# Optimization experiments

Measured on AMD Instinct MI355X. Metric: run time of the kernel, lower is better.

Reference implementation:

```python
import jax, jax.numpy as jnp
import numpy as np

TOP_K = 8
NUM_GROUPS = 8


def setup_inputs() -> dict:
    key = jax.random.key(0)
    ks = jax.random.split(key, 6)
    T_B, T_S, H, I, E, G = 1, 2048, 2048, 768, 32, NUM_GROUPS
    hidden_states = jax.random.normal(ks[0], (T_B, T_S, H), dtype=jnp.float32)
    gate_weight = jax.random.normal(ks[1], (E, H), dtype=jnp.float32) * 0.02
    gate_up_proj = jax.random.normal(ks[2], (E, 2 * I, H), dtype=jnp.float32) * 0.02
    down_proj = jax.random.normal(ks[3], (E, H, I), dtype=jnp.float32) * 0.02
    merge_groups = jax.random.randint(ks[4], (E,), 0, G, dtype=jnp.int64)
    # ensure every group id appears at least once so dominant experts are well-defined
    merge_groups = merge_groups.at[:G].set(jnp.arange(G, dtype=jnp.int64))
    dominant_experts = jax.random.randint(ks[5], (G,), 0, E, dtype=jnp.int64)
    return {
        "hidden_states": hidden_states,
        "gate_weight": gate_weight,
        "gate_up_proj": gate_up_proj,
        "down_proj": down_proj,
        "merge_groups": merge_groups,
        "dominant_experts": dominant_experts,
    }


def reference(hidden_states, gate_weight, gate_up_proj, down_proj, merge_groups, dominant_experts):
    B, S, H = hidden_states.shape
    G = dominant_experts.shape[0]
    x = hidden_states.reshape(-1, H)  # [T, H]

    # Router: softmax over all experts, then top-k of the probabilities (as in source)
    logits = jnp.einsum("th,eh->te", x, gate_weight)
    probs = jax.nn.softmax(logits.astype(jnp.float32), axis=-1).astype(logits.dtype)
    top_val, top_idx = jax.lax.top_k(probs, TOP_K)  # [T, K]
    top_val = top_val / jnp.sum(top_val, axis=-1, keepdims=True)  # norm_topk_prob

    # Each selected expert e is replaced by its group's dominant expert; by linearity
    # of the scatter-add combine, sum routing weights per (token, group).
    sel_group = merge_groups[top_idx]  # [T, K] in [0, G)
    onehot = jax.nn.one_hot(sel_group, G, dtype=top_val.dtype)  # [T, K, G]
    w_tg = jnp.einsum("tk,tkg->tg", top_val, onehot)  # combined weight per token/group

    gu = gate_up_proj[dominant_experts]  # [G, 2I, H]
    dn = down_proj[dominant_experts]     # [G, H, I]

    h = jnp.einsum("th,goh->tgo", x, gu)           # [T, G, 2I]
    gate, up = jnp.split(h, 2, axis=-1)              # [T, G, I] each
    act = jax.nn.silu(gate) * up                     # SwiGLU
    y = jnp.einsum("tgi,ghi->tgh", act, dn)        # [T, G, H]
    out = jnp.einsum("tg,tgh->th", w_tg, y)        # combine
    return out.reshape(B, S, H)
```

## Files before the change

### kernel.cpp

```cpp
#include <hip/hip_runtime.h>
#include <hip/hip_bf16.h>

typedef __attribute__((ext_vector_type(8))) short short8v;
typedef __attribute__((ext_vector_type(4))) float f32x4;

#define T_TOK 2048
#define HDIM  2048
#define IDIM  768
#define NEXP  32
#define NGRP  8

__device__ __forceinline__ unsigned short f2b(float f){
  unsigned u = __float_as_uint(f);
  u = u + 0x7FFFu + ((u >> 16) & 1u);
  return (unsigned short)(u >> 16);
}
__device__ __forceinline__ float b2f(unsigned short s){
  return __uint_as_float(((unsigned)s) << 16);
}

__global__ __launch_bounds__(256) void router_kernel(
    const float* __restrict__ x, const float* __restrict__ gw,
    const int* __restrict__ mg, float* __restrict__ wtg,
    unsigned short* __restrict__ xb)
{
  __shared__ float xs[4][2048];
  __shared__ float lg[4][32];
  int tid = threadIdx.x;
  int t0 = blockIdx.x * 4;

  #pragma unroll
  for (int k = 0; k < 8; k++){
    int idx = k*256 + tid;
    int tok = idx >> 9, wi = idx & 511;
    float4 v = ((const float4*)(x + (size_t)(t0 + tok)*HDIM))[wi];
    ((float4*)xs[tok])[wi] = v;
    ushort4 b; b.x=f2b(v.x); b.y=f2b(v.y); b.z=f2b(v.z); b.w=f2b(v.w);
    ((ushort4*)(xb + (size_t)(t0+tok)*HDIM))[wi] = b;
  }
  __syncthreads();

  int e = tid >> 3, ch = tid & 7;
  float s0=0.f, s1=0.f, s2=0.f, s3=0.f;
  const float4* gv = (const float4*)(gw + (size_t)e*HDIM);
  #pragma unroll 4
  for (int k = 0; k < 64; k++){
    int i4 = ch + 8*k;
    float4 b  = gv[i4];
    float4 a0 = ((const float4*)xs[0])[i4];
    float4 a1 = ((const float4*)xs[1])[i4];
    float4 a2 = ((const float4*)xs[2])[i4];
    float4 a3 = ((const float4*)xs[3])[i4];
    s0 += a0.x*b.x + a0.y*b.y + a0.z*b.z + a0.w*b.w;
    s1 += a1.x*b.x + a1.y*b.y + a1.z*b.z + a1.w*b.w;
    s2 += a2.x*b.x + a2.y*b.y + a2.z*b.z + a2.w*b.w;
    s3 += a3.x*b.x + a3.y*b.y + a3.z*b.z + a3.w*b.w;
  }
  #pragma unroll
  for (int off=1; off<8; off<<=1){
    s0 += __shfl_xor(s0, off); s1 += __shfl_xor(s1, off);
    s2 += __shfl_xor(s2, off); s3 += __shfl_xor(s3, off);
  }
  if (ch == 0){ lg[0][e]=s0; lg[1][e]=s1; lg[2][e]=s2; lg[3][e]=s3; }
  __syncthreads();

  int wv = tid >> 6, lane = tid & 63;
  float val = (lane < 32) ? lg[wv][lane] : -1e30f;
  float mx = val;
  #pragma unroll
  for (int off=16; off; off>>=1) mx = fmaxf(mx, __shfl_xor(mx, off));
  float p = (lane < 32) ? expf(val - mx) : 0.f;
  float sm = p;
  #pragma unroll
  for (int off=16; off; off>>=1) sm += __shfl_xor(sm, off);
  float v = (lane < 32) ? (p / sm) : -1.f;
  int idx = lane;
  float vals[8]; int idxs[8];
  #pragma unroll
  for (int it=0; it<8; it++){
    float bv = v; int bi = idx;
    #pragma unroll
    for (int off=32; off; off>>=1){
      float ov = __shfl_xor(bv, off); int oi = __shfl_xor(bi, off);
      if (ov > bv || (ov == bv && oi < bi)){ bv = ov; bi = oi; }
    }
    vals[it] = bv; idxs[it] = bi;
    if (lane == bi) v = -1.f;
  }
  float tot = vals[0]+vals[1]+vals[2]+vals[3]+vals[4]+vals[5]+vals[6]+vals[7];
  float racc = 0.f;
  #pragma unroll
  for (int it=0; it<8; it++){
    int grp = mg[idxs[it]];
    if (lane == grp) racc += vals[it] / tot;
  }
  if (lane < 8) wtg[(size_t)(t0+wv)*NGRP + lane] = racc;
}

__global__ __launch_bounds__(256) void convert_kernel(
    const float* __restrict__ src, unsigned short* __restrict__ dst,
    const int* __restrict__ de, size_t per_expert)
{
  int g = blockIdx.z;
  size_t i4 = (size_t)blockIdx.x*256 + threadIdx.x;
  const float4* s = (const float4*)(src + (size_t)de[g]*per_expert);
  float4 vv = s[i4];
  ushort4 b; b.x=f2b(vv.x); b.y=f2b(vv.y); b.z=f2b(vv.z); b.w=f2b(vv.w);
  ((ushort4*)(dst + (size_t)g*per_expert))[i4] = b;
}

__device__ __forceinline__ void stage128x32(const unsigned short* g,
                                            int ld, unsigned short* lds, int tid)
{
  int w = tid >> 6;
  const unsigned short* g0 = g + (size_t)(tid >> 2)*ld + (tid & 3)*8;
  const unsigned short* g1 = g0 + (size_t)64*ld;
  __builtin_amdgcn_global_load_lds((const __attribute__((address_space(1))) void*)g0,
      (__attribute__((address_space(3))) void*)(lds + w*512), 16, 0, 0);
  __builtin_amdgcn_global_load_lds((const __attribute__((address_space(1))) void*)g1,
      (__attribute__((address_space(3))) void*)(lds + 2048 + w*512), 16, 0, 0);
}

__device__ __forceinline__ void frag_mma(const unsigned short* As,
                                         const unsigned short* Bs,
                                         f32x4 acc[4][4], int lane, int wr, int wc)
{
  int fr = lane & 15, kk = (lane >> 4) * 8;
  short8v a[4], b[4];
  #pragma unroll
  for (int m=0;m<4;m++) a[m] = *(const short8v*)(As + (wr*64 + m*16 + fr)*32 + kk);
  #pragma unroll
  for (int n=0;n<4;n++) b[n] = *(const short8v*)(Bs + (wc*64 + n*16 + fr)*32 + kk);
  #pragma unroll
  for (int m=0;m<4;m++){
    #pragma unroll
    for (int n=0;n<4;n++){
      acc[m][n] = __builtin_amdgcn_mfma_f32_16x16x32_bf16(a[m], b[n], acc[m][n], 0, 0, 0);
    }
  }
}

__global__ __launch_bounds__(256, 2) void gemm1_kernel(
    const unsigned short* __restrict__ xb, const unsigned short* __restrict__ gu,
    unsigned short* __restrict__ hb)
{
  __shared__ unsigned short As[4096], Bs[4096];
  int tid = threadIdx.x, lane = tid & 63, w = tid >> 6, wr = w >> 1, wc = w & 1;
  int m0 = blockIdx.x*128, n0 = blockIdx.y*128, g = blockIdx.z;
  const unsigned short* Ab = xb + (size_t)m0*HDIM;
  const unsigned short* Bb = gu + ((size_t)g*1536 + n0)*HDIM;
  f32x4 zero = {0.f,0.f,0.f,0.f};
  f32x4 acc[4][4];
  #pragma unroll
  for (int m=0;m<4;m++){ acc[m][0]=zero; acc[m][1]=zero; acc[m][2]=zero; acc[m][3]=zero; }
  for (int k0=0; k0<HDIM; k0+=32){
    __syncthreads();
    stage128x32(Ab + k0, HDIM, As, tid);
    stage128x32(Bb + k0, HDIM, Bs, tid);
    __syncthreads();
    frag_mma(As, Bs, acc, lane, wr, wc);
  }
  int col = lane & 15, r0 = (lane >> 4) * 4;
  unsigned short* C = hb + (size_t)g*T_TOK*1536;
  #pragma unroll
  for (int m=0;m<4;m++){
    int row = m0 + wr*64 + m*16 + r0;
    #pragma unroll
    for (int n=0;n<4;n++){
      int cc = n0 + wc*64 + n*16 + col;
      #pragma unroll
      for (int j=0;j<4;j++) C[(size_t)(row + j)*1536 + cc] = f2b(acc[m][n][j]);
    }
  }
}

__global__ __launch_bounds__(256) void swiglu_kernel(
    const unsigned short* __restrict__ hb, const float* __restrict__ wtg,
    unsigned short* __restrict__ actb)
{
  int cid = blockIdx.x*256 + threadIdx.x;
  int g = cid / 196608;
  int rem = cid - g*196608;
  int t = rem / 96;
  int c = rem - t*96;
  const unsigned short* row = hb + ((size_t)g*T_TOK + t)*1536;
  short8v g8 = *(const short8v*)(row + c*8);
  short8v u8 = *(const short8v*)(row + 768 + c*8);
  float wv = wtg[(size_t)t*NGRP + g];
  short8v r;
  #pragma unroll
  for (int j=0;j<8;j++){
    float gf = b2f((unsigned short)g8[j]);
    float uf = b2f((unsigned short)u8[j]);
    float sg = gf / (1.f + expf(-gf));
    r[j] = (short)f2b(sg * uf * wv);
  }
  *(short8v*)(actb + ((size_t)g*T_TOK + t)*IDIM + c*8) = r;
}

__global__ __launch_bounds__(256, 2) void gemm2_kernel(
    const unsigned short* __restrict__ actb, const unsigned short* __restrict__ dnb,
    float* __restrict__ part)
{
  __shared__ unsigned short As[4096], Bs[4096];
  int tid = threadIdx.x, lane = tid & 63, w = tid >> 6, wr = w >> 1, wc = w & 1;
  int m0 = blockIdx.x*128, n0 = blockIdx.y*128, z = blockIdx.z;
  f32x4 zero = {0.f,0.f,0.f,0.f};
  f32x4 acc[4][4];
  #pragma unroll
  for (int m=0;m<4;m++){ acc[m][0]=zero; acc[m][1]=zero; acc[m][2]=zero; acc[m][3]=zero; }
  for (int gg=0; gg<2; gg++){
    int g = z*2 + gg;
    const unsigned short* Ab = actb + ((size_t)g*T_TOK + m0)*IDIM;
    const unsigned short* Bb = dnb  + ((size_t)g*HDIM  + n0)*IDIM;
    for (int k0=0; k0<IDIM; k0+=32){
      __syncthreads();
      stage128x32(Ab + k0, IDIM, As, tid);
      stage128x32(Bb + k0, IDIM, Bs, tid);
      __syncthreads();
      frag_mma(As, Bs, acc, lane, wr, wc);
    }
  }
  int col = lane & 15, r0 = (lane >> 4) * 4;
  float* C = part + (size_t)z*T_TOK*HDIM;
  #pragma unroll
  for (int m=0;m<4;m++){
    int row = m0 + wr*64 + m*16 + r0;
    #pragma unroll
    for (int n=0;n<4;n++){
      int cc = n0 + wc*64 + n*16 + col;
      #pragma unroll
      for (int j=0;j<4;j++) C[(size_t)(row + j)*HDIM + cc] = acc[m][n][j];
    }
  }
}

__global__ __launch_bounds__(256) void reduce_kernel(
    const float* __restrict__ p, float* __restrict__ o)
{
  size_t i = ((size_t)blockIdx.x*256 + threadIdx.x)*4;
  float4 a0 = *(const float4*)(p + i);
  float4 a1 = *(const float4*)(p + 4194304 + i);
  float4 a2 = *(const float4*)(p + 8388608 + i);
  float4 a3 = *(const float4*)(p + 12582912 + i);
  float4 r;
  r.x = a0.x + a1.x + a2.x + a3.x;
  r.y = a0.y + a1.y + a2.y + a3.y;
  r.z = a0.z + a1.z + a2.z + a3.z;
  r.w = a0.w + a1.w + a2.w + a3.w;
  *(float4*)(o + i) = r;
}

extern "C" void kernel_launch(void* const* d_in, const int* in_sizes, int n_in,
                              void* d_out, int out_size, void* d_ws, size_t ws_size,
                              hipStream_t stream)
{
  (void)in_sizes; (void)n_in; (void)out_size; (void)ws_size;
  const float* x   = (const float*)d_in[0];
  const float* gw  = (const float*)d_in[1];
  const float* gup = (const float*)d_in[2];
  const float* dnp = (const float*)d_in[3];
  const int*   mg  = (const int*)d_in[4];
  const int*   de  = (const int*)d_in[5];
  float* out = (float*)d_out;
  char* ws = (char*)d_ws;

  float*          wtg  = (float*)(ws + 0);
  unsigned short* xb   = (unsigned short*)(ws + 65536);
  unsigned short* dnb  = (unsigned short*)(ws + 8454144);
  unsigned short* actb = (unsigned short*)(ws + 33619968);
  unsigned short* gub  = (unsigned short*)(ws + 58785792);
  unsigned short* hb   = (unsigned short*)(ws + 109117440);
  float*          part = (float*)(ws + 58785792);

  router_kernel<<<512, 256, 0, stream>>>(x, gw, mg, wtg, xb);
  convert_kernel<<<dim3(3072,1,8), 256, 0, stream>>>(gup, gub, de, (size_t)1536*2048);
  convert_kernel<<<dim3(1536,1,8), 256, 0, stream>>>(dnp, dnb, de, (size_t)2048*768);
  gemm1_kernel<<<dim3(16,12,8), 256, 0, stream>>>(xb, gub, hb);
  swiglu_kernel<<<6144, 256, 0, stream>>>(hb, wtg, actb);
  gemm2_kernel<<<dim3(16,16,4), 256, 0, stream>>>(actb, dnb, part);
  reduce_kernel<<<4096, 256, 0, stream>>>(part, out);
}
```

Before: 287.9 us.

## Rewrite both GEMMs as 256x256-tile double-buffered pipelined kernels with swizzled LDS

Both expert GEMMs move from 128x128 tiles with a K step of 32 and full syncs to 256x256 tiles with 8 waves and a K step of 64. The LDS is double-buffered and XOR-swizzled, and global-to-LDS loads for the next K-tile are interleaved across four MFMA phases using vmcnt waits and raw barriers, with s_setprio raised around MFMA bursts. The aim is to hide global load latency, cut LDS bank conflicts and raise arithmetic intensity per block. The trade-off is 128 KB of LDS per block, which makes the declared 2 blocks per CU unlikely, 128 accumulator registers per thread, and far fewer blocks (384 for gemm1 and 256 for gemm2), which could underfill 256 CUs.

```diff
diff --git a/kernel.cpp b/kernel.cpp
--- a/kernel.cpp
+++ b/kernel.cpp
@@ -109,67 +109,155 @@
   ((ushort4*)(dst + (size_t)g*per_expert))[i4] = b;
 }
 
-__device__ __forceinline__ void stage128x32(const unsigned short* g,
-                                            int ld, unsigned short* lds, int tid)
-{
-  int w = tid >> 6;
-  const unsigned short* g0 = g + (size_t)(tid >> 2)*ld + (tid & 3)*8;
-  const unsigned short* g1 = g0 + (size_t)64*ld;
-  __builtin_amdgcn_global_load_lds((const __attribute__((address_space(1))) void*)g0,
-      (__attribute__((address_space(3))) void*)(lds + w*512), 16, 0, 0);
-  __builtin_amdgcn_global_load_lds((const __attribute__((address_space(1))) void*)g1,
-      (__attribute__((address_space(3))) void*)(lds + 2048 + w*512), 16, 0, 0);
-}
-
-__device__ __forceinline__ void frag_mma(const unsigned short* As,
-                                         const unsigned short* Bs,
-                                         f32x4 acc[4][4], int lane, int wr, int wc)
-{
-  int fr = lane & 15, kk = (lane >> 4) * 8;
-  short8v a[4], b[4];
-  #pragma unroll
-  for (int m=0;m<4;m++) a[m] = *(const short8v*)(As + (wr*64 + m*16 + fr)*32 + kk);
-  #pragma unroll
-  for (int n=0;n<4;n++) b[n] = *(const short8v*)(Bs + (wc*64 + n*16 + fr)*32 + kk);
-  #pragma unroll
-  for (int m=0;m<4;m++){
+
+__device__ __forceinline__ void stage_half_g(
+    const unsigned short* __restrict__ gsrc, int ldElems,
+    unsigned short* __restrict__ ldsHalf, int tid)
+{
+  int rl0 = tid >> 3;
+  int cb  = (tid & 7) * 16;
+  int w   = tid >> 6;
+  #pragma unroll
+  for (int j = 0; j < 2; j++){
+    int rl  = j*64 + rl0;
+    int scb = cb ^ ((rl & 4) << 3);
+    const unsigned short* src = gsrc + (size_t)rl*ldElems + (scb >> 1);
+    __builtin_amdgcn_global_load_lds(
+        (const __attribute__((address_space(1))) void*)src,
+        (__attribute__((address_space(3))) void*)(ldsHalf + j*4096 + w*512),
+        16, 0, 0);
+  }
+}
+
+template<int P>
+__device__ __forceinline__ void read_a_frags(const unsigned short* Ab,
+                                             short8v (&a)[4][2], int fr, int colOff)
+{
+  #pragma unroll
+  for (int i=0;i<4;i++){
+    const char* rb = (const char*)Ab + (size_t)(((P*4+i)*16 + fr)*128);
+    a[i][0] = *(const short8v*)(rb + colOff);
+    a[i][1] = *(const short8v*)(rb + 64 + colOff);
+  }
+}
+
+__device__ __forceinline__ void read_b_frags(const unsigned short* Bb,
+                                             short8v (&b)[2][2], int wn, int fr, int colOff)
+{
+  #pragma unroll
+  for (int n=0;n<2;n++){
+    const char* rb = (const char*)Bb + (size_t)((wn*32 + n*16 + fr)*128);
+    b[n][0] = *(const short8v*)(rb + colOff);
+    b[n][1] = *(const short8v*)(rb + 64 + colOff);
+  }
+}
+
+template<int P>
+__device__ __forceinline__ void mfma_phase(const short8v (&a)[4][2],
+                                           const short8v (&b)[2][2],
+                                           f32x4 (&acc)[16][2])
+{
+  __builtin_amdgcn_s_setprio(1);
+  #pragma unroll
+  for (int i=0;i<4;i++){
     #pragma unroll
-    for (int n=0;n<4;n++){
-      acc[m][n] = __builtin_amdgcn_mfma_f32_16x16x32_bf16(a[m], b[n], acc[m][n], 0, 0, 0);
+    for (int n=0;n<2;n++){
+      acc[P*4+i][n] = __builtin_amdgcn_mfma_f32_16x16x32_bf16(a[i][0], b[n][0], acc[P*4+i][n], 0,0,0);
+      acc[P*4+i][n] = __builtin_amdgcn_mfma_f32_16x16x32_bf16(a[i][1], b[n][1], acc[P*4+i][n], 0,0,0);
     }
   }
-}
-
-__global__ __launch_bounds__(256, 2) void gemm1_kernel(
+  __builtin_amdgcn_s_setprio(0);
+}
+
+#define BARRIER() do { __builtin_amdgcn_s_barrier(); __builtin_amdgcn_sched_barrier(0); } while(0)
+#define WAITV(N)  asm volatile("s_waitcnt vmcnt(" #N ")" ::: "memory")
+
+__global__ __launch_bounds__(512, 2) void gemm1_kernel(
     const unsigned short* __restrict__ xb, const unsigned short* __restrict__ gu,
     unsigned short* __restrict__ hb)
 {
-  __shared__ unsigned short As[4096], Bs[4096];
-  int tid = threadIdx.x, lane = tid & 63, w = tid >> 6, wr = w >> 1, wc = w & 1;
-  int m0 = blockIdx.x*128, n0 = blockIdx.y*128, g = blockIdx.z;
-  const unsigned short* Ab = xb + (size_t)m0*HDIM;
-  const unsigned short* Bb = gu + ((size_t)g*1536 + n0)*HDIM;
-  f32x4 zero = {0.f,0.f,0.f,0.f};
-  f32x4 acc[4][4];
-  #pragma unroll
-  for (int m=0;m<4;m++){ acc[m][0]=zero; acc[m][1]=zero; acc[m][2]=zero; acc[m][3]=zero; }
-  for (int k0=0; k0<HDIM; k0+=32){
-    __syncthreads();
-    stage128x32(Ab + k0, HDIM, As, tid);
-    stage128x32(Bb + k0, HDIM, Bs, tid);
-    __syncthreads();
-    frag_mma(As, Bs, acc, lane, wr, wc);
-  }
-  int col = lane & 15, r0 = (lane >> 4) * 4;
-  unsigned short* C = hb + (size_t)g*T_TOK*1536;
-  #pragma unroll
-  for (int m=0;m<4;m++){
-    int row = m0 + wr*64 + m*16 + r0;
+  __shared__ unsigned short Al[2][16384];
+  __shared__ unsigned short Bl[2][16384];
+  int tid = threadIdx.x, lane = tid & 63, wn = tid >> 6;
+  int fr = lane & 15;
+  int colOff = ((lane >> 4) * 16) ^ ((lane & 4) << 3);
+  int m0 = blockIdx.x * 256, n0 = blockIdx.y * 256, g = blockIdx.z;
+  const unsigned short* Abase = xb + (size_t)m0 * HDIM;
+  const unsigned short* Bbase = gu + ((size_t)g * 1536 + n0) * HDIM;
+
+  f32x4 acc[16][2];
+  #pragma unroll
+  for (int m=0;m<16;m++){ acc[m][0] = (f32x4){0,0,0,0}; acc[m][1] = (f32x4){0,0,0,0}; }
+  short8v bfrag[2][2];
+
+  #define STG1(buf, unit, kt2) do { \
+    if ((unit)==0)      stage_half_g(Bbase + (size_t)(kt2)*64,                   HDIM, &Bl[buf][0],    tid); \
+    else if ((unit)==1) stage_half_g(Bbase + (size_t)128*HDIM + (size_t)(kt2)*64,HDIM, &Bl[buf][8192], tid); \
+    else if ((unit)==2) stage_half_g(Abase + (size_t)(kt2)*64,                   HDIM, &Al[buf][0],    tid); \
+    else                stage_half_g(Abase + (size_t)128*HDIM + (size_t)(kt2)*64,HDIM, &Al[buf][8192], tid); \
+  } while(0)
+
+  STG1(0,0,0); STG1(0,1,0); STG1(0,2,0); STG1(0,3,0);
+  WAITV(3);
+  BARRIER();
+
+  for (int kt = 0; kt < 31; ++kt){
+    const unsigned short* Ab = Al[kt & 1];
+    const unsigned short* Bb = Bl[kt & 1];
+    int nb = (kt + 1) & 1, k2 = kt + 1;
+    { short8v a[4][2]; read_a_frags<0>(Ab, a, fr, colOff);
+      read_b_frags(Bb, bfrag, wn, fr, colOff);
+      STG1(nb, 0, k2);
+      WAITV(4); BARRIER();
+      mfma_phase<0>(a, bfrag, acc);
+      BARRIER(); }
+    { short8v a[4][2]; read_a_frags<1>(Ab, a, fr, colOff);
+      STG1(nb, 1, k2);
+      WAITV(5); BARRIER();
+      mfma_phase<1>(a, bfrag, acc);
+      BARRIER(); }
+    { short8v a[4][2]; read_a_frags<2>(Ab, a, fr, colOff);
+      STG1(nb, 2, k2);
+      WAITV(6); BARRIER();
+      mfma_phase<2>(a, bfrag, acc);
+      BARRIER(); }
+    { short8v a[4][2]; read_a_frags<3>(Ab, a, fr, colOff);
+      STG1(nb, 3, k2);
+      WAITV(3); BARRIER();
+      mfma_phase<3>(a, bfrag, acc);
+      BARRIER(); }
+  }
+  {
+    const unsigned short* Ab = Al[1];
+    const unsigned short* Bb = Bl[1];
+    { short8v a[4][2]; read_a_frags<0>(Ab, a, fr, colOff);
+      read_b_frags(Bb, bfrag, wn, fr, colOff);
+      WAITV(2); BARRIER();
+      mfma_phase<0>(a, bfrag, acc);
+      BARRIER(); }
+    { short8v a[4][2]; read_a_frags<1>(Ab, a, fr, colOff);
+      WAITV(1); BARRIER();
+      mfma_phase<1>(a, bfrag, acc);
+      BARRIER(); }
+    { short8v a[4][2]; read_a_frags<2>(Ab, a, fr, colOff);
+      WAITV(0); BARRIER();
+      mfma_phase<2>(a, bfrag, acc);
+      BARRIER(); }
+    { short8v a[4][2]; read_a_frags<3>(Ab, a, fr, colOff);
+      mfma_phase<3>(a, bfrag, acc); }
+  }
+  #undef STG1
+
+  unsigned short* Cb = hb + (size_t)g * T_TOK * 1536;
+  int r0 = (lane >> 4) * 4, c0 = n0 + wn * 32 + fr;
+  #pragma unroll
+  for (int m = 0; m < 16; m++){
     #pragma unroll
-    for (int n=0;n<4;n++){
-      int cc = n0 + wc*64 + n*16 + col;
+    for (int n = 0; n < 2; n++){
       #pragma unroll
-      for (int j=0;j<4;j++) C[(size_t)(row + j)*1536 + cc] = f2b(acc[m][n][j]);
+      for (int j = 0; j < 4; j++){
+        Cb[(size_t)(m0 + m*16 + r0 + j) * 1536 + (c0 + n*16)] = f2b(acc[m][n][j]);
+      }
     }
   }
 }
@@ -198,39 +286,95 @@
   *(short8v*)(actb + ((size_t)g*T_TOK + t)*IDIM + c*8) = r;
 }
 
-__global__ __launch_bounds__(256, 2) void gemm2_kernel(
+__global__ __launch_bounds__(512, 2) void gemm2_kernel(
     const unsigned short* __restrict__ actb, const unsigned short* __restrict__ dnb,
     float* __restrict__ part)
 {
-  __shared__ unsigned short As[4096], Bs[4096];
-  int tid = threadIdx.x, lane = tid & 63, w = tid >> 6, wr = w >> 1, wc = w & 1;
-  int m0 = blockIdx.x*128, n0 = blockIdx.y*128, z = blockIdx.z;
-  f32x4 zero = {0.f,0.f,0.f,0.f};
-  f32x4 acc[4][4];
-  #pragma unroll
-  for (int m=0;m<4;m++){ acc[m][0]=zero; acc[m][1]=zero; acc[m][2]=zero; acc[m][3]=zero; }
-  for (int gg=0; gg<2; gg++){
-    int g = z*2 + gg;
-    const unsigned short* Ab = actb + ((size_t)g*T_TOK + m0)*IDIM;
-    const unsigned short* Bb = dnb  + ((size_t)g*HDIM  + n0)*IDIM;
-    for (int k0=0; k0<IDIM; k0+=32){
-      __syncthreads();
-      stage128x32(Ab + k0, IDIM, As, tid);
-      stage128x32(Bb + k0, IDIM, Bs, tid);
-      __syncthreads();
-      frag_mma(As, Bs, acc, lane, wr, wc);
-    }
-  }
-  int col = lane & 15, r0 = (lane >> 4) * 4;
-  float* C = part + (size_t)z*T_TOK*HDIM;
-  #pragma unroll
-  for (int m=0;m<4;m++){
-    int row = m0 + wr*64 + m*16 + r0;
+  __shared__ unsigned short Al[2][16384];
+  __shared__ unsigned short Bl[2][16384];
+  int tid = threadIdx.x, lane = tid & 63, wn = tid >> 6;
+  int fr = lane & 15;
+  int colOff = ((lane >> 4) * 16) ^ ((lane & 4) << 3);
+  int m0 = blockIdx.x * 256, n0 = blockIdx.y * 256, z = blockIdx.z;
+
+  f32x4 acc[16][2];
+  #pragma unroll
+  for (int m=0;m<16;m++){ acc[m][0] = (f32x4){0,0,0,0}; acc[m][1] = (f32x4){0,0,0,0}; }
+  short8v bfrag[2][2];
+
+  #define STG2(buf, unit, kt2) do { \
+    int gi = ((kt2) >= 12) ? 1 : 0; \
+    int gg = z*2 + gi; \
+    int kk = ((kt2) - gi*12) * 64; \
+    const unsigned short* Aseg = actb + (size_t)(gg*T_TOK + m0)*IDIM + kk; \
+    const unsigned short* Bseg = dnb  + (size_t)(gg*HDIM + n0)*IDIM + kk; \
+    if ((unit)==0)      stage_half_g(Bseg,                      IDIM, &Bl[buf][0],    tid); \
+    else if ((unit)==1) stage_half_g(Bseg + (size_t)128*IDIM,   IDIM, &Bl[buf][8192], tid); \
+    else if ((unit)==2) stage_half_g(Aseg,                      IDIM, &Al[buf][0],    tid); \
+    else                stage_half_g(Aseg + (size_t)128*IDIM,   IDIM, &Al[buf][8192], tid); \
+  } while(0)
+
+  STG2(0,0,0); STG2(0,1,0); STG2(0,2,0); STG2(0,3,0);
+  WAITV(3);
+  BARRIER();
+
+  for (int kt = 0; kt < 23; ++kt){
+    const unsigned short* Ab = Al[kt & 1];
+    const unsigned short* Bb = Bl[kt & 1];
+    int nb = (kt + 1) & 1, k2 = kt + 1;
+    { short8v a[4][2]; read_a_frags<0>(Ab, a, fr, colOff);
+      read_b_frags(Bb, bfrag, wn, fr, colOff);
+      STG2(nb, 0, k2);
+      WAITV(4); BARRIER();
+      mfma_phase<0>(a, bfrag, acc);
+      BARRIER(); }
+    { short8v a[4][2]; read_a_frags<1>(Ab, a, fr, colOff);
+      STG2(nb, 1, k2);
+      WAITV(5); BARRIER();
+      mfma_phase<1>(a, bfrag, acc);
+      BARRIER(); }
+    { short8v a[4][2]; read_a_frags<2>(Ab, a, fr, colOff);
+      STG2(nb, 2, k2);
+      WAITV(6); BARRIER();
+      mfma_phase<2>(a, bfrag, acc);
+      BARRIER(); }
+    { short8v a[4][2]; read_a_frags<3>(Ab, a, fr, colOff);
+      STG2(nb, 3, k2);
+      WAITV(3); BARRIER();
+      mfma_phase<3>(a, bfrag, acc);
+      BARRIER(); }
+  }
+  {
+    const unsigned short* Ab = Al[1];
+    const unsigned short* Bb = Bl[1];
+    { short8v a[4][2]; read_a_frags<0>(Ab, a, fr, colOff);
+      read_b_frags(Bb, bfrag, wn, fr, colOff);
+      WAITV(2); BARRIER();
+      mfma_phase<0>(a, bfrag, acc);
+      BARRIER(); }
+    { short8v a[4][2]; read_a_frags<1>(Ab, a, fr, colOff);
+      WAITV(1); BARRIER();
+      mfma_phase<1>(a, bfrag, acc);
+      BARRIER(); }
+    { short8v a[4][2]; read_a_frags<2>(Ab, a, fr, colOff);
+      WAITV(0); BARRIER();
+      mfma_phase<2>(a, bfrag, acc);
+      BARRIER(); }
+    { short8v a[4][2]; read_a_frags<3>(Ab, a, fr, colOff);
+      mfma_phase<3>(a, bfrag, acc); }
+  }
+  #undef STG2
+
+  float* Cb = part + (size_t)z * T_TOK * HDIM;
+  int r0 = (lane >> 4) * 4, c0 = n0 + wn * 32 + fr;
+  #pragma unroll
+  for (int m = 0; m < 16; m++){
     #pragma unroll
-    for (int n=0;n<4;n++){
-      int cc = n0 + wc*64 + n*16 + col;
+    for (int n = 0; n < 2; n++){
       #pragma unroll
-      for (int j=0;j<4;j++) C[(size_t)(row + j)*HDIM + cc] = acc[m][n][j];
+      for (int j = 0; j < 4; j++){
+        Cb[(size_t)(m0 + m*16 + r0 + j) * HDIM + (c0 + n*16)] = acc[m][n][j];
+      }
     }
   }
 }
@@ -276,8 +420,8 @@
   router_kernel<<<512, 256, 0, stream>>>(x, gw, mg, wtg, xb);
   convert_kernel<<<dim3(3072,1,8), 256, 0, stream>>>(gup, gub, de, (size_t)1536*2048);
   convert_kernel<<<dim3(1536,1,8), 256, 0, stream>>>(dnp, dnb, de, (size_t)2048*768);
-  gemm1_kernel<<<dim3(16,12,8), 256, 0, stream>>>(xb, gub, hb);
+  gemm1_kernel<<<dim3(8,6,8), 512, 0, stream>>>(xb, gub, hb);
   swiglu_kernel<<<6144, 256, 0, stream>>>(hb, wtg, actb);
-  gemm2_kernel<<<dim3(16,16,4), 256, 0, stream>>>(actb, dnb, part);
+  gemm2_kernel<<<dim3(8,8,4), 512, 0, stream>>>(actb, dnb, part);
   reduce_kernel<<<4096, 256, 0, stream>>>(part, out);
 }
```

After: 287.1 us. Within noise of the previous version (-0.3%).

## Fuse SwiGLU into gemm1 epilogue and rewrite GEMMs with double-buffered 256x256 tiles

Applied to the files above, without the earlier changes.

The gate/up weight conversion now interleaves gate and up rows in 16-row chunks, so each gemm1 tile holds matching gate and up columns. This lets SwiGLU and the routing weight be applied in the gemm1 epilogue, which removes the intermediate hb tensor and the separate swiglu kernel. Both GEMMs move to 512-thread blocks with 256x256 tiles, 64-wide K steps, XOR-swizzled LDS, double-buffered global-to-LDS loads overlapped with MFMA, and raised wave priority around the MFMA sections. The cost is higher register and LDS use per block and fewer blocks in the grid, which may limit occupancy.

```diff
diff --git a/kernel.cpp b/kernel.cpp
--- a/kernel.cpp
+++ b/kernel.cpp
@@ -7,7 +7,6 @@
 #define T_TOK 2048
 #define HDIM  2048
 #define IDIM  768
-#define NEXP  32
 #define NGRP  8
 
 __device__ __forceinline__ unsigned short f2b(float f){
@@ -97,140 +96,234 @@
   if (lane < 8) wtg[(size_t)(t0+wv)*NGRP + lane] = racc;
 }
 
-__global__ __launch_bounds__(256) void convert_kernel(
+__global__ __launch_bounds__(256) void convert_gu_kernel(
     const float* __restrict__ src, unsigned short* __restrict__ dst,
-    const int* __restrict__ de, size_t per_expert)
+    const int* __restrict__ de)
+{
+  int g = blockIdx.z;
+  int i4 = blockIdx.x*256 + threadIdx.x;
+  int j  = i4 >> 9;
+  int c4 = i4 & 511;
+  int q = j >> 5, r = j & 31;
+  int srow = (r < 16) ? (q*16 + r) : (768 + q*16 + (r - 16));
+  const float4* s = (const float4*)(src + ((size_t)de[g]*1536 + srow)*HDIM);
+  float4 vv = s[c4];
+  ushort4 b; b.x=f2b(vv.x); b.y=f2b(vv.y); b.z=f2b(vv.z); b.w=f2b(vv.w);
+  ((ushort4*)(dst + ((size_t)g*1536 + j)*HDIM))[c4] = b;
+}
+
+__global__ __launch_bounds__(256) void convert_dn_kernel(
+    const float* __restrict__ src, unsigned short* __restrict__ dst,
+    const int* __restrict__ de)
 {
   int g = blockIdx.z;
   size_t i4 = (size_t)blockIdx.x*256 + threadIdx.x;
-  const float4* s = (const float4*)(src + (size_t)de[g]*per_expert);
+  const float4* s = (const float4*)(src + (size_t)de[g]*1572864);
   float4 vv = s[i4];
   ushort4 b; b.x=f2b(vv.x); b.y=f2b(vv.y); b.z=f2b(vv.z); b.w=f2b(vv.w);
-  ((ushort4*)(dst + (size_t)g*per_expert))[i4] = b;
-}
-
-__device__ __forceinline__ void stage128x32(const unsigned short* g,
-                                            int ld, unsigned short* lds, int tid)
-{
-  int w = tid >> 6;
-  const unsigned short* g0 = g + (size_t)(tid >> 2)*ld + (tid & 3)*8;
-  const unsigned short* g1 = g0 + (size_t)64*ld;
-  __builtin_amdgcn_global_load_lds((const __attribute__((address_space(1))) void*)g0,
-      (__attribute__((address_space(3))) void*)(lds + w*512), 16, 0, 0);
-  __builtin_amdgcn_global_load_lds((const __attribute__((address_space(1))) void*)g1,
-      (__attribute__((address_space(3))) void*)(lds + 2048 + w*512), 16, 0, 0);
-}
-
-__device__ __forceinline__ void frag_mma(const unsigned short* As,
-                                         const unsigned short* Bs,
-                                         f32x4 acc[4][4], int lane, int wr, int wc)
-{
-  int fr = lane & 15, kk = (lane >> 4) * 8;
-  short8v a[4], b[4];
-  #pragma unroll
-  for (int m=0;m<4;m++) a[m] = *(const short8v*)(As + (wr*64 + m*16 + fr)*32 + kk);
-  #pragma unroll
-  for (int n=0;n<4;n++) b[n] = *(const short8v*)(Bs + (wc*64 + n*16 + fr)*32 + kk);
-  #pragma unroll
-  for (int m=0;m<4;m++){
+  ((ushort4*)(dst + (size_t)g*1572864))[i4] = b;
+}
+
+
+__device__ __forceinline__ void stage_half_g(
+    const unsigned short* __restrict__ gsrc, int ldElems,
+    unsigned short* __restrict__ ldsHalf, int tid)
+{
+  int rl0 = tid >> 3;
+  int cb  = (tid & 7) * 16;
+  int w   = tid >> 6;
+  #pragma unroll
+  for (int j = 0; j < 2; j++){
+    int rl  = j*64 + rl0;
+    int scb = cb ^ ((rl & 7) << 4);
+    const unsigned short* src = gsrc + (size_t)rl*ldElems + (scb >> 1);
+    __builtin_amdgcn_global_load_lds(
+        (const __attribute__((address_space(1))) void*)src,
+        (__attribute__((address_space(3))) void*)(ldsHalf + j*4096 + w*512),
+        16, 0, 0);
+  }
+}
+
+__device__ __forceinline__ void read_b4(const unsigned short* Bb,
+                                        short8v (&b)[4][2], int wn, int fr, int colOff)
+{
+  #pragma unroll
+  for (int n=0;n<4;n++){
+    const char* rb = (const char*)Bb + (size_t)((wn*64 + n*16 + fr)*128);
+    b[n][0] = *(const short8v*)(rb + colOff);
+    b[n][1] = *(const short8v*)(rb + (colOff ^ 64));
+  }
+}
+
+template<int P>
+__device__ __forceinline__ void subphase(const unsigned short* Ab, int wm, int fr, int colOff,
+                                         const short8v (&b)[4][2], f32x4 (&acc)[8][4])
+{
+  short8v a[2][2];
+  #pragma unroll
+  for (int i=0;i<2;i++){
+    const char* rb = (const char*)Ab + (size_t)((wm*128 + (P*2+i)*16 + fr)*128);
+    a[i][0] = *(const short8v*)(rb + colOff);
+    a[i][1] = *(const short8v*)(rb + (colOff ^ 64));
+  }
+  __builtin_amdgcn_s_setprio(1);
+  #pragma unroll
+  for (int i=0;i<2;i++){
     #pragma unroll
     for (int n=0;n<4;n++){
-      acc[m][n] = __builtin_amdgcn_mfma_f32_16x16x32_bf16(a[m], b[n], acc[m][n], 0, 0, 0);
+      acc[P*2+i][n] = __builtin_amdgcn_mfma_f32_16x16x32_bf16(a[i][0], b[n][0], acc[P*2+i][n],0,0,0);
+      acc[P*2+i][n] = __builtin_amdgcn_mfma_f32_16x16x32_bf16(a[i][1], b[n][1], acc[P*2+i][n],0,0,0);
     }
   }
-}
-
-__global__ __launch_bounds__(256, 2) void gemm1_kernel(
+  __builtin_amdgcn_s_setprio(0);
+}
+
+#define WAITV(N)  asm volatile("s_waitcnt vmcnt(" #N ")" ::: "memory")
+
+__global__ __launch_bounds__(512, 2) void gemm1_kernel(
     const unsigned short* __restrict__ xb, const unsigned short* __restrict__ gu,
-    unsigned short* __restrict__ hb)
-{
-  __shared__ unsigned short As[4096], Bs[4096];
-  int tid = threadIdx.x, lane = tid & 63, w = tid >> 6, wr = w >> 1, wc = w & 1;
-  int m0 = blockIdx.x*128, n0 = blockIdx.y*128, g = blockIdx.z;
-  const unsigned short* Ab = xb + (size_t)m0*HDIM;
-  const unsigned short* Bb = gu + ((size_t)g*1536 + n0)*HDIM;
-  f32x4 zero = {0.f,0.f,0.f,0.f};
-  f32x4 acc[4][4];
-  #pragma unroll
-  for (int m=0;m<4;m++){ acc[m][0]=zero; acc[m][1]=zero; acc[m][2]=zero; acc[m][3]=zero; }
-  for (int k0=0; k0<HDIM; k0+=32){
-    __syncthreads();
-    stage128x32(Ab + k0, HDIM, As, tid);
-    stage128x32(Bb + k0, HDIM, Bs, tid);
-    __syncthreads();
-    frag_mma(As, Bs, acc, lane, wr, wc);
-  }
-  int col = lane & 15, r0 = (lane >> 4) * 4;
-  unsigned short* C = hb + (size_t)g*T_TOK*1536;
-  #pragma unroll
-  for (int m=0;m<4;m++){
-    int row = m0 + wr*64 + m*16 + r0;
-    #pragma unroll
-    for (int n=0;n<4;n++){
-      int cc = n0 + wc*64 + n*16 + col;
+    const float* __restrict__ wtg, unsigned short* __restrict__ actb)
+{
+  __shared__ unsigned short Al[2][16384];
+  __shared__ unsigned short Bl[2][16384];
+  int tid = threadIdx.x, lane = tid & 63, w = tid >> 6;
+  int wm = w >> 2, wn = w & 3;
+  int fr = lane & 15;
+  int colOff = ((lane >> 4) * 16) ^ ((fr & 7) << 4);
+  int bid = blockIdx.x;
+  int P = bid % 48, mb = bid / 48;
+  int m0 = mb * 256, n0 = (P % 6) * 256, g = P / 6;
+  const unsigned short* Abase = xb + (size_t)m0 * HDIM;
+  const unsigned short* Bbase = gu + ((size_t)g * 1536 + n0) * HDIM;
+
+  f32x4 acc[8][4];
+  #pragma unroll
+  for (int m=0;m<8;m++){
+    #pragma unroll
+    for (int n=0;n<4;n++) acc[m][n] = (f32x4){0,0,0,0};
+  }
+  short8v b[4][2];
+
+  #define STG1(buf, kt2) do { \
+    stage_half_g(Bbase + (size_t)(kt2)*64,                    HDIM, &Bl[buf][0],    tid); \
+    stage_half_g(Bbase + (size_t)128*HDIM + (size_t)(kt2)*64, HDIM, &Bl[buf][8192], tid); \
+    stage_half_g(Abase + (size_t)(kt2)*64,                    HDIM, &Al[buf][0],    tid); \
+    stage_half_g(Abase + (size_t)128*HDIM + (size_t)(kt2)*64, HDIM, &Al[buf][8192], tid); \
+  } while(0)
+
+  STG1(0, 0);
+  WAITV(0);
+  __builtin_amdgcn_s_barrier();
+
+  for (int kt = 0; kt < 31; ++kt){
+    int cur = kt & 1, nb = cur ^ 1;
+    STG1(nb, kt+1);
+    __builtin_amdgcn_sched_barrier(0);
+    read_b4(Bl[cur], b, wn, fr, colOff);
+    subphase<0>(Al[cur], wm, fr, colOff, b, acc);
+    subphase<1>(Al[cur], wm, fr, colOff, b, acc);
+    subphase<2>(Al[cur], wm, fr, colOff, b, acc);
+    subphase<3>(Al[cur], wm, fr, colOff, b, acc);
+    WAITV(0);
+    __builtin_amdgcn_s_barrier();
+  }
+  read_b4(Bl[1], b, wn, fr, colOff);
+  subphase<0>(Al[1], wm, fr, colOff, b, acc);
+  subphase<1>(Al[1], wm, fr, colOff, b, acc);
+  subphase<2>(Al[1], wm, fr, colOff, b, acc);
+  subphase<3>(Al[1], wm, fr, colOff, b, acc);
+  #undef STG1
+
+  int r0 = (lane >> 4) * 4;
+  int qbase = (n0 + wn * 64) >> 5;
+  #pragma unroll
+  for (int mi = 0; mi < 8; mi++){
+    int trow = m0 + wm*128 + mi*16 + r0;
+    #pragma unroll
+    for (int q = 0; q < 2; q++){
+      int icol = (qbase + q)*16 + fr;
       #pragma unroll
-      for (int j=0;j<4;j++) C[(size_t)(row + j)*1536 + cc] = f2b(acc[m][n][j]);
+      for (int j = 0; j < 4; j++){
+        int t = trow + j;
+        float wv = wtg[(size_t)t*NGRP + g];
+        float gf = acc[mi][2*q][j];
+        float uf = acc[mi][2*q+1][j];
+        float sg = gf / (1.f + expf(-gf));
+        actb[((size_t)g*T_TOK + t)*IDIM + icol] = f2b(sg * uf * wv);
+      }
     }
   }
 }
 
-__global__ __launch_bounds__(256) void swiglu_kernel(
-    const unsigned short* __restrict__ hb, const float* __restrict__ wtg,
-    unsigned short* __restrict__ actb)
-{
-  int cid = blockIdx.x*256 + threadIdx.x;
-  int g = cid / 196608;
-  int rem = cid - g*196608;
-  int t = rem / 96;
-  int c = rem - t*96;
-  const unsigned short* row = hb + ((size_t)g*T_TOK + t)*1536;
-  short8v g8 = *(const short8v*)(row + c*8);
-  short8v u8 = *(const short8v*)(row + 768 + c*8);
-  float wv = wtg[(size_t)t*NGRP + g];
-  short8v r;
-  #pragma unroll
-  for (int j=0;j<8;j++){
-    float gf = b2f((unsigned short)g8[j]);
-    float uf = b2f((unsigned short)u8[j]);
-    float sg = gf / (1.f + expf(-gf));
-    r[j] = (short)f2b(sg * uf * wv);
-  }
-  *(short8v*)(actb + ((size_t)g*T_TOK + t)*IDIM + c*8) = r;
-}
-
-__global__ __launch_bounds__(256, 2) void gemm2_kernel(
+__global__ __launch_bounds__(512, 2) void gemm2_kernel(
     const unsigned short* __restrict__ actb, const unsigned short* __restrict__ dnb,
     float* __restrict__ part)
 {
-  __shared__ unsigned short As[4096], Bs[4096];
-  int tid = threadIdx.x, lane = tid & 63, w = tid >> 6, wr = w >> 1, wc = w & 1;
-  int m0 = blockIdx.x*128, n0 = blockIdx.y*128, z = blockIdx.z;
-  f32x4 zero = {0.f,0.f,0.f,0.f};
-  f32x4 acc[4][4];
-  #pragma unroll
-  for (int m=0;m<4;m++){ acc[m][0]=zero; acc[m][1]=zero; acc[m][2]=zero; acc[m][3]=zero; }
-  for (int gg=0; gg<2; gg++){
-    int g = z*2 + gg;
-    const unsigned short* Ab = actb + ((size_t)g*T_TOK + m0)*IDIM;
-    const unsigned short* Bb = dnb  + ((size_t)g*HDIM  + n0)*IDIM;
-    for (int k0=0; k0<IDIM; k0+=32){
-      __syncthreads();
-      stage128x32(Ab + k0, IDIM, As, tid);
-      stage128x32(Bb + k0, IDIM, Bs, tid);
-      __syncthreads();
-      frag_mma(As, Bs, acc, lane, wr, wc);
-    }
-  }
-  int col = lane & 15, r0 = (lane >> 4) * 4;
-  float* C = part + (size_t)z*T_TOK*HDIM;
-  #pragma unroll
-  for (int m=0;m<4;m++){
-    int row = m0 + wr*64 + m*16 + r0;
-    #pragma unroll
-    for (int n=0;n<4;n++){
-      int cc = n0 + wc*64 + n*16 + col;
+  __shared__ unsigned short Al[2][16384];
+  __shared__ unsigned short Bl[2][16384];
+  int tid = threadIdx.x, lane = tid & 63, w = tid >> 6;
+  int wm = w >> 2, wn = w & 3;
+  int fr = lane & 15;
+  int colOff = ((lane >> 4) * 16) ^ ((fr & 7) << 4);
+  int bid = blockIdx.x;
+  int P = bid % 32, mb = bid / 32;
+  int m0 = mb * 256, n0 = (P % 8) * 256, z = P / 8;
+
+  f32x4 acc[8][4];
+  #pragma unroll
+  for (int m=0;m<8;m++){
+    #pragma unroll
+    for (int n=0;n<4;n++) acc[m][n] = (f32x4){0,0,0,0};
+  }
+  short8v b[4][2];
+
+  #define STG2(buf, kt2) do { \
+    int gi = ((kt2) >= 12) ? 1 : 0; \
+    int gg = z*2 + gi; \
+    int kk = ((kt2) - gi*12) * 64; \
+    const unsigned short* Aseg = actb + (size_t)(gg*T_TOK + m0)*IDIM + kk; \
+    const unsigned short* Bseg = dnb  + (size_t)(gg*HDIM + n0)*IDIM + kk; \
+    stage_half_g(Bseg,                    IDIM, &Bl[buf][0],    tid); \
+    stage_half_g(Bseg + (size_t)128*IDIM, IDIM, &Bl[buf][8192], tid); \
+    stage_half_g(Aseg,                    IDIM, &Al[buf][0],    tid); \
+    stage_half_g(Aseg + (size_t)128*IDIM, IDIM, &Al[buf][8192], tid); \
+  } while(0)
+
+  STG2(0, 0);
+  WAITV(0);
+  __builtin_amdgcn_s_barrier();
+
+  for (int kt = 0; kt < 23; ++kt){
+    int cur = kt & 1, nb = cur ^ 1;
+    STG2(nb, kt+1);
+    __builtin_amdgcn_sched_barrier(0);
+    read_b4(Bl[cur], b, wn, fr, colOff);
+    subphase<0>(Al[cur], wm, fr, colOff, b, acc);
+    subphase<1>(Al[cur], wm, fr, colOff, b, acc);
+    subphase<2>(Al[cur], wm, fr, colOff, b, acc);
+    subphase<3>(Al[cur], wm, fr, colOff, b, acc);
+    WAITV(0);
+    __builtin_amdgcn_s_barrier();
+  }
+  read_b4(Bl[1], b, wn, fr, colOff);
+  subphase<0>(Al[1], wm, fr, colOff, b, acc);
+  subphase<1>(Al[1], wm, fr, colOff, b, acc);
+  subphase<2>(Al[1], wm, fr, colOff, b, acc);
+  subphase<3>(Al[1], wm, fr, colOff, b, acc);
+  #undef STG2
+
+  float* Cb = part + (size_t)z * T_TOK * HDIM;
+  int r0 = (lane >> 4) * 4;
+  #pragma unroll
+  for (int mi = 0; mi < 8; mi++){
+    int row = m0 + wm*128 + mi*16 + r0;
+    #pragma unroll
+    for (int n = 0; n < 4; n++){
+      int cc = n0 + wn*64 + n*16 + fr;
       #pragma unroll
-      for (int j=0;j<4;j++) C[(size_t)(row + j)*HDIM + cc] = acc[m][n][j];
+      for (int j = 0; j < 4; j++){
+        Cb[(size_t)(row + j)*HDIM + cc] = acc[mi][n][j];
+      }
     }
   }
 }
@@ -269,15 +362,13 @@
   unsigned short* xb   = (unsigned short*)(ws + 65536);
   unsigned short* dnb  = (unsigned short*)(ws + 8454144);
   unsigned short* actb = (unsigned short*)(ws + 33619968);
+  float*          part = (float*)(ws + 58785792);
   unsigned short* gub  = (unsigned short*)(ws + 58785792);
-  unsigned short* hb   = (unsigned short*)(ws + 109117440);
-  float*          part = (float*)(ws + 58785792);
 
   router_kernel<<<512, 256, 0, stream>>>(x, gw, mg, wtg, xb);
-  convert_kernel<<<dim3(3072,1,8), 256, 0, stream>>>(gup, gub, de, (size_t)1536*2048);
-  convert_kernel<<<dim3(1536,1,8), 256, 0, stream>>>(dnp, dnb, de, (size_t)2048*768);
-  gemm1_kernel<<<dim3(16,12,8), 256, 0, stream>>>(xb, gub, hb);
-  swiglu_kernel<<<6144, 256, 0, stream>>>(hb, wtg, actb);
-  gemm2_kernel<<<dim3(16,16,4), 256, 0, stream>>>(actb, dnb, part);
+  convert_gu_kernel<<<dim3(3072,1,8), 256, 0, stream>>>(gup, gub, de);
+  convert_dn_kernel<<<dim3(1536,1,8), 256, 0, stream>>>(dnp, dnb, de);
+  gemm1_kernel<<<384, 512, 0, stream>>>(xb, gub, wtg, actb);
+  gemm2_kernel<<<256, 512, 0, stream>>>(actb, dnb, part);
   reduce_kernel<<<4096, 256, 0, stream>>>(part, out);
 }
```

New measurement: 261.7 us. 1.1x faster.
